# Kernel tuning notes

Hardware: AMD Instinct MI355X
Metric: run time of the kernel (lower is better)

Reference implementation:

```python
import jax, jax.numpy as jnp
import numpy as np

DIM = 512
HEADS = 8
DIM_HEAD = 64
HIDDEN = HEADS * DIM_HEAD  # 512
B, N, M = 4, 2048, 2048


def setup_inputs() -> dict:
    key = jax.random.key(0)
    ks = jax.random.split(key, 7)
    s = 0.02
    return {
        "x": jax.random.normal(ks[0], (B, N, DIM), jnp.float32),
        "context": jax.random.normal(ks[1], (B, M, DIM), jnp.float32),
        "Wq": jax.random.normal(ks[2], (DIM, HIDDEN), jnp.float32) * s,
        "Wk": jax.random.normal(ks[3], (DIM, HIDDEN), jnp.float32) * s,
        "Wv": jax.random.normal(ks[4], (DIM, HIDDEN), jnp.float32) * s,
        "Wo": jax.random.normal(ks[5], (HIDDEN, DIM), jnp.float32) * s,
        "bo": jnp.zeros((DIM,), jnp.float32),
    }


def reference(x, context, Wq, Wk, Wv, Wo, bo):
    scale = DIM_HEAD ** (-0.5)
    # projections: [B, N, HIDDEN] -> [B, H, N, D]
    def split_heads(t):
        b, n, _ = t.shape
        return t.reshape(b, n, HEADS, DIM_HEAD).transpose(0, 2, 1, 3)
    q = split_heads(x @ Wq)
    k = split_heads(context @ Wk)
    v = split_heads(context @ Wv)
    # scores: [B, H, N, M]
    sim = jnp.einsum('bhid,bhjd->bhij', q, k) * scale
    attn = jax.nn.softmax(sim, axis=-1)
    out = jnp.einsum('bhij,bhjd->bhid', attn, v)  # [B, H, N, D]
    out = out.transpose(0, 2, 1, 3).reshape(x.shape[0], x.shape[1], HIDDEN)
    return out @ Wo + bo
```

## Files before the change

kernel.cpp:

```cpp
#include <hip/hip_runtime.h>
#include <hip/hip_bf16.h>


typedef __attribute__((ext_vector_type(8))) short bf16x8;
typedef __attribute__((ext_vector_type(4))) float f32x4;

#define MFMA16(a, b, c) __builtin_amdgcn_mfma_f32_16x16x32_bf16(a, b, c, 0, 0, 0)
#define SCALE_LOG2E 0.18033688011112042f

static __device__ inline unsigned short f2b(float f) {
    __hip_bfloat16 h = __float2bfloat16(f);
    return __builtin_bit_cast(unsigned short, h);
}
static __device__ inline unsigned int pk_rnd(float hi, float lo) {
    unsigned uh = __builtin_bit_cast(unsigned, hi) + 0x8000u;
    unsigned ul = __builtin_bit_cast(unsigned, lo) + 0x8000u;
    return __builtin_amdgcn_perm(uh, ul, 0x07060302);
}
static __device__ inline void gll16(const void* g, void* l) {
    __builtin_amdgcn_global_load_lds(
        (const __attribute__((address_space(1))) void*)g,
        (__attribute__((address_space(3))) void*)l, 16, 0, 0);
}

__global__ __launch_bounds__(256) void prep_kernel(const float* __restrict__ x,
                                                   const float* __restrict__ ctx,
                                                   const float* __restrict__ Wq,
                                                   const float* __restrict__ Wk,
                                                   const float* __restrict__ Wv,
                                                   const float* __restrict__ Wo,
                                                   unsigned short* __restrict__ xb,
                                                   unsigned short* __restrict__ cb,
                                                   unsigned short* __restrict__ wt_base) {
    __shared__ float T[64][65];
    const int bid = blockIdx.x, tid = threadIdx.x;
    if (bid < 8192) {
        const float* src = (bid < 4096) ? x : ctx;
        unsigned short* dst = (bid < 4096) ? xb : cb;
        int i = (bid & 4095) * 256 + tid;
        const float4 v = reinterpret_cast<const float4*>(src)[i];
        uint2 o;
        o.x = pk_rnd(v.y, v.x);
        o.y = pk_rnd(v.w, v.z);
        reinterpret_cast<uint2*>(dst)[i] = o;
        return;
    }
    const int b = bid - 8192;
    const int which = b >> 6, t6 = b & 63;
    const float* W = (which == 0) ? Wq : (which == 1) ? Wk : (which == 2) ? Wv : Wo;
    unsigned short* Wt = wt_base + (size_t)which * 512 * 512;
    const int n0 = (t6 & 7) * 64, k0 = (t6 >> 3) * 64;
    const int rr = tid >> 4, cc = (tid & 15) * 4;
    #pragma unroll
    for (int i = 0; i < 4; i++) {
        const float4 v = *reinterpret_cast<const float4*>(&W[(size_t)(k0 + rr + 16 * i) * 512 + n0 + cc]);
        T[rr + 16 * i][cc + 0] = v.x; T[rr + 16 * i][cc + 1] = v.y;
        T[rr + 16 * i][cc + 2] = v.z; T[rr + 16 * i][cc + 3] = v.w;
    }
    __syncthreads();
    #pragma unroll
    for (int i = 0; i < 4; i++) {
        int n = rr + 16 * i;
        uint2 o;
        o.x = pk_rnd(T[cc + 1][n], T[cc + 0][n]);
        o.y = pk_rnd(T[cc + 3][n], T[cc + 2][n]);
        *reinterpret_cast<uint2*>(&Wt[(size_t)(n0 + n) * 512 + k0 + cc]) = o;
    }
}

__device__ inline void gemm_tile_128(const unsigned short* __restrict__ A,
                                     const unsigned short* __restrict__ Bt,
                                     int row0, int col0, f32x4 acc[4][4]) {
    __shared__ unsigned short As[128 * 32];
    __shared__ unsigned short Bs[128 * 32];
    const int tid  = threadIdx.x;
    const int lane = tid & 63, wave = tid >> 6;
    const int quad = lane >> 4, mr = lane & 15;
    const int m_off = (wave & 1) * 64, n_off = (wave >> 1) * 64;

    const int lrow = lane >> 2;
    const int lq   = (lane & 3) ^ (lrow & 3);
    const unsigned short* aSrc = A  + (size_t)(row0 + wave * 32 + lrow) * 512 + lq * 8;
    const unsigned short* bSrc = Bt + (size_t)(col0 + wave * 32 + lrow) * 512 + lq * 8;
    unsigned short* aL0 = &As[(wave * 32) * 32];
    unsigned short* aL1 = &As[(wave * 32 + 16) * 32];
    unsigned short* bL0 = &Bs[(wave * 32) * 32];
    unsigned short* bL1 = &Bs[(wave * 32 + 16) * 32];

    for (int kt = 0; kt < 16; kt++) {
        __syncthreads();
        gll16(aSrc + kt * 32, aL0);
        gll16(aSrc + 16 * 512 + kt * 32, aL1);
        gll16(bSrc + kt * 32, bL0);
        gll16(bSrc + 16 * 512 + kt * 32, bL1);
        __syncthreads();
        bf16x8 af[4], bfr[4];
        #pragma unroll
        for (int i = 0; i < 4; i++) {
            int m = m_off + i * 16 + mr;
            af[i] = *reinterpret_cast<const bf16x8*>(&As[m * 32 + ((quad ^ (m & 3)) * 8)]);
        }
        #pragma unroll
        for (int j = 0; j < 4; j++) {
            int n = n_off + j * 16 + mr;
            bfr[j] = *reinterpret_cast<const bf16x8*>(&Bs[n * 32 + ((quad ^ (n & 3)) * 8)]);
        }
        #pragma unroll
        for (int i = 0; i < 4; i++)
            #pragma unroll
            for (int j = 0; j < 4; j++)
                acc[i][j] = MFMA16(af[i], bfr[j], acc[i][j]);
    }
}

__global__ __launch_bounds__(256) void gemm_proj_kernel(const unsigned short* __restrict__ xb,
                                                        const unsigned short* __restrict__ cb,
                                                        const unsigned short* __restrict__ wt_base,
                                                        unsigned short* __restrict__ qkv_base) {
    const int f = blockIdx.x, g = f & 7, j = f >> 3;
    const int xt = j & 3;
    const int ry = g + 8 * ((j >> 2) & 7);
    const int which = j >> 5;

    const unsigned short* A  = (which == 0) ? xb : cb;
    const unsigned short* Bt = wt_base + (size_t)which * 512 * 512;
    unsigned short* out      = qkv_base + (size_t)which * 8192 * 512;

    f32x4 acc[4][4];
    #pragma unroll
    for (int i = 0; i < 4; i++)
        #pragma unroll
        for (int j2 = 0; j2 < 4; j2++) acc[i][j2] = (f32x4){0.f, 0.f, 0.f, 0.f};

    gemm_tile_128(A, Bt, ry * 128, xt * 128, acc);

    const int lane = threadIdx.x & 63, wave = threadIdx.x >> 6;
    const int quad = lane >> 4, mr = lane & 15;
    const int m_off = (wave & 1) * 64, n_off = (wave >> 1) * 64;
    const float qs = (which == 0) ? SCALE_LOG2E : 1.0f;

    if (which == 2) {
        #pragma unroll
        for (int i = 0; i < 4; i++) {
            #pragma unroll
            for (int j2 = 0; j2 < 4; j2++) {
                int gcol = xt * 128 + n_off + j2 * 16 + mr;
                int h = gcol >> 6, d = gcol & 63;
                #pragma unroll
                for (int r = 0; r < 4; r++) {
                    int grow = ry * 128 + m_off + i * 16 + quad * 4 + r;
                    int b = grow >> 11, n = grow & 2047;
                    out[((size_t)(b * 8 + h) * 64 + d) * 2048 + n] = f2b(acc[i][j2][r]);
                }
            }
        }
    } else {
        #pragma unroll
        for (int i = 0; i < 4; i++) {
            #pragma unroll
            for (int j2 = 0; j2 < 4; j2++) {
                int gcol = xt * 128 + n_off + j2 * 16 + mr;
                int h = gcol >> 6, d = gcol & 63;
                #pragma unroll
                for (int r = 0; r < 4; r++) {
                    int grow = ry * 128 + m_off + i * 16 + quad * 4 + r;
                    int b = grow >> 11, n = grow & 2047;
                    out[((size_t)(b * 8 + h) * 2048 + n) * 64 + d] = f2b(acc[i][j2][r] * qs);
                }
            }
        }
    }
}

__global__ __launch_bounds__(256) void flash_kernel(const unsigned short* __restrict__ qw,
                                                    const unsigned short* __restrict__ kw,
                                                    const unsigned short* __restrict__ vt,
                                                    float* __restrict__ p0,
                                                    float* __restrict__ p1,
                                                    float* __restrict__ l0,
                                                    float* __restrict__ l1) {
    __shared__ unsigned short Ks[64 * 72];
    __shared__ unsigned short Vs[64 * 72];
    __shared__ unsigned short Pw[4][32 * 72];

    const int f = blockIdx.x, g = f & 7, j = f >> 3;
    const int qtile = j & 15;
    const int kidx  = (j >> 4) & 1;
    const int bh    = g + 8 * (j >> 5);

    const int tid  = threadIdx.x;
    const int lane = tid & 63, wave = tid >> 6;
    const int quad = lane >> 4, mr = lane & 15;

    const unsigned short* qbase = qw + ((size_t)bh * 2048 + qtile * 128 + wave * 32) * 64;
    const unsigned short* kbase = kw + (size_t)bh * 2048 * 64;
    const unsigned short* vbase = vt + (size_t)bh * 64 * 2048;
    float* Pdst = kidx ? p1 : p0;
    float* ldst = kidx ? l1 : l0;

    bf16x8 qf[2][2];
    #pragma unroll
    for (int gq = 0; gq < 2; gq++) {
        qf[gq][0] = *reinterpret_cast<const bf16x8*>(qbase + (gq * 16 + mr) * 64 + quad * 8);
        qf[gq][1] = *reinterpret_cast<const bf16x8*>(qbase + (gq * 16 + mr) * 64 + 32 + quad * 8);
    }

    bf16x8 ones;
    #pragma unroll
    for (int e = 0; e < 8; e++) ones[e] = (short)0x3F80;

    f32x4 oacc[2][4], lacc[2];
    #pragma unroll
    for (int gq = 0; gq < 2; gq++) {
        lacc[gq] = (f32x4){0.f, 0.f, 0.f, 0.f};
        #pragma unroll
        for (int nt = 0; nt < 4; nt++) oacc[gq][nt] = (f32x4){0.f, 0.f, 0.f, 0.f};
    }

    const int srow = tid >> 2, soff = (tid & 3) * 16;

    const int kbeg = kidx * 1024;
    for (int key0 = kbeg; key0 < kbeg + 1024; key0 += 64) {
        __syncthreads();
        {
            const uint4* kp = reinterpret_cast<const uint4*>(kbase + (size_t)(key0 + srow) * 64 + soff);
            uint4* kd = reinterpret_cast<uint4*>(&Ks[srow * 72 + soff]);
            kd[0] = kp[0]; kd[1] = kp[1];
            const uint4* vp = reinterpret_cast<const uint4*>(vbase + (size_t)srow * 2048 + key0 + soff);
            uint4* vd = reinterpret_cast<uint4*>(&Vs[srow * 72 + soff]);
            vd[0] = vp[0]; vd[1] = vp[1];
        }
        __syncthreads();

        f32x4 sv[2][4];
        #pragma unroll
        for (int gq = 0; gq < 2; gq++)
            #pragma unroll
            for (int kt = 0; kt < 4; kt++) sv[gq][kt] = (f32x4){0.f, 0.f, 0.f, 0.f};
        #pragma unroll
        for (int c = 0; c < 2; c++) {
            #pragma unroll
            for (int kt = 0; kt < 4; kt++) {
                bf16x8 kf = *reinterpret_cast<const bf16x8*>(&Ks[(kt * 16 + mr) * 72 + c * 32 + quad * 8]);
                sv[0][kt] = MFMA16(kf, qf[0][c], sv[0][kt]);
                sv[1][kt] = MFMA16(kf, qf[1][c], sv[1][kt]);
            }
        }

        #pragma unroll
        for (int gq = 0; gq < 2; gq++) {
            #pragma unroll
            for (int kt = 0; kt < 4; kt++) {
                uint2 w;
                w.x = pk_rnd(__builtin_exp2f(sv[gq][kt][1]), __builtin_exp2f(sv[gq][kt][0]));
                w.y = pk_rnd(__builtin_exp2f(sv[gq][kt][3]), __builtin_exp2f(sv[gq][kt][2]));
                *reinterpret_cast<uint2*>(&Pw[wave][(gq * 16 + mr) * 72 + kt * 16 + quad * 4]) = w;
            }
        }
        asm volatile("s_waitcnt lgkmcnt(0)" ::: "memory");

        #pragma unroll
        for (int ks = 0; ks < 2; ks++) {
            bf16x8 pf0 = *reinterpret_cast<const bf16x8*>(&Pw[wave][(mr) * 72 + ks * 32 + quad * 8]);
            bf16x8 pf1 = *reinterpret_cast<const bf16x8*>(&Pw[wave][(16 + mr) * 72 + ks * 32 + quad * 8]);
            lacc[0] = MFMA16(pf0, ones, lacc[0]);
            lacc[1] = MFMA16(pf1, ones, lacc[1]);
            #pragma unroll
            for (int nt = 0; nt < 4; nt++) {
                bf16x8 vf = *reinterpret_cast<const bf16x8*>(&Vs[(nt * 16 + mr) * 72 + ks * 32 + quad * 8]);
                oacc[0][nt] = MFMA16(pf0, vf, oacc[0][nt]);
                oacc[1][nt] = MFMA16(pf1, vf, oacc[1][nt]);
            }
        }
    }

    const int b = bh >> 3, h = bh & 7;
    #pragma unroll
    for (int gq = 0; gq < 2; gq++) {
        #pragma unroll
        for (int nt = 0; nt < 4; nt++) {
            #pragma unroll
            for (int r = 0; r < 4; r++) {
                int row = qtile * 128 + wave * 32 + gq * 16 + quad * 4 + r;
                Pdst[((size_t)b * 2048 + row) * 512 + h * 64 + nt * 16 + mr] = oacc[gq][nt][r];
            }
        }
        if (mr == 0) {
            #pragma unroll
            for (int r = 0; r < 4; r++) {
                int row = qtile * 128 + wave * 32 + gq * 16 + quad * 4 + r;
                ldst[(size_t)bh * 2048 + row] = lacc[gq][r];
            }
        }
    }
}

__global__ __launch_bounds__(256) void combine_kernel(const float* __restrict__ p0,
                                                      const float* __restrict__ p1,
                                                      const float* __restrict__ l0,
                                                      const float* __restrict__ l1,
                                                      unsigned short* __restrict__ ob) {
    const int idx = blockIdx.x * 256 + threadIdx.x;
    const size_t flat = (size_t)idx * 4;
    const int row = (int)(flat >> 9);
    const int c   = (int)(flat & 511);
    const int bh  = (row >> 11) * 8 + (c >> 6);
    const int qn  = row & 2047;
    const float lv = l0[(size_t)bh * 2048 + qn] + l1[(size_t)bh * 2048 + qn];
    const float li = 1.0f / lv;
    const float4 a = reinterpret_cast<const float4*>(p0)[idx];
    const float4 bb = reinterpret_cast<const float4*>(p1)[idx];
    uint2 o;
    o.x = pk_rnd((a.y + bb.y) * li, (a.x + bb.x) * li);
    o.y = pk_rnd((a.w + bb.w) * li, (a.z + bb.z) * li);
    reinterpret_cast<uint2*>(ob)[idx] = o;
}

__global__ __launch_bounds__(256) void gemm_out_kernel(const unsigned short* __restrict__ obuf,
                                                       const unsigned short* __restrict__ Wot,
                                                       const float* __restrict__ bo,
                                                       float* __restrict__ out) {
    const int f = blockIdx.x, g = f & 7, j = f >> 3;
    const int xt = j & 3;
    const int ry = g + 8 * (j >> 2);

    f32x4 acc[4][4];
    #pragma unroll
    for (int i = 0; i < 4; i++)
        #pragma unroll
        for (int j2 = 0; j2 < 4; j2++) acc[i][j2] = (f32x4){0.f, 0.f, 0.f, 0.f};

    gemm_tile_128(obuf, Wot, ry * 128, xt * 128, acc);

    const int lane = threadIdx.x & 63, wave = threadIdx.x >> 6;
    const int quad = lane >> 4, mr = lane & 15;
    const int m_off = (wave & 1) * 64, n_off = (wave >> 1) * 64;
    #pragma unroll
    for (int i = 0; i < 4; i++) {
        #pragma unroll
        for (int j2 = 0; j2 < 4; j2++) {
            int gcol = xt * 128 + n_off + j2 * 16 + mr;
            float bias = bo[gcol];
            #pragma unroll
            for (int r = 0; r < 4; r++) {
                int grow = ry * 128 + m_off + i * 16 + quad * 4 + r;
                out[(size_t)grow * 512 + gcol] = acc[i][j2][r] + bias;
            }
        }
    }
}

extern "C" void kernel_launch(void* const* d_in, const int* in_sizes, int n_in,
                              void* d_out, int out_size, void* d_ws, size_t ws_size,
                              hipStream_t stream) {
    const float* x   = (const float*)d_in[0];
    const float* ctx = (const float*)d_in[1];
    const float* Wq  = (const float*)d_in[2];
    const float* Wk  = (const float*)d_in[3];
    const float* Wv  = (const float*)d_in[4];
    const float* Wo  = (const float*)d_in[5];
    const float* bo  = (const float*)d_in[6];
    float* out = (float*)d_out;

    unsigned short* ws  = (unsigned short*)d_ws;
    unsigned short* xb  = ws;
    unsigned short* cb  = xb + (size_t)8192 * 512;
    unsigned short* Wt  = cb + (size_t)8192 * 512;
    unsigned short* qkv = Wt + (size_t)4 * 512 * 512;
    unsigned short* ob  = qkv + (size_t)3 * 8192 * 512;

    float* p0 = out;
    float* p1 = (float*)xb;
    float* l0 = (float*)Wt;
    float* l1 = (float*)(Wt + (size_t)512 * 512);

    prep_kernel<<<8448, 256, 0, stream>>>(x, ctx, Wq, Wk, Wv, Wo, xb, cb, Wt);
    gemm_proj_kernel<<<768, 256, 0, stream>>>(xb, cb, Wt, qkv);
    flash_kernel<<<1024, 256, 0, stream>>>(qkv, qkv + (size_t)8192 * 512,
                                           qkv + (size_t)2 * 8192 * 512, p0, p1, l0, l1);
    combine_kernel<<<4096, 256, 0, stream>>>(p0, p1, l0, l1, ob);
    gemm_out_kernel<<<256, 256, 0, stream>>>(ob, Wt + (size_t)3 * 512 * 512, bo, out);
}
```

Measured before the change: 194.5 us.

## Load K/V fragments directly from global into registers, drop LDS staging and barriers

The flash kernel no longer stages K and V tiles through shared memory with two barriers per iteration. Each wave now loads its own MFMA fragments straight from global memory into registers, and a minimum-occupancy hint is added to the launch bounds. Separately, the V-transpose projection epilogue packs four bf16 values into one 8-byte store instead of four scalar stores. The loader change removes block-wide synchronisation and LDS traffic, but each of the four waves now re-reads the same K/V data from global memory or cache and raises register pressure.

```diff
diff --git a/kernel.cpp b/kernel.cpp
--- a/kernel.cpp
+++ b/kernel.cpp
@@ -146,12 +146,12 @@
             for (int j2 = 0; j2 < 4; j2++) {
                 int gcol = xt * 128 + n_off + j2 * 16 + mr;
                 int h = gcol >> 6, d = gcol & 63;
-                #pragma unroll
-                for (int r = 0; r < 4; r++) {
-                    int grow = ry * 128 + m_off + i * 16 + quad * 4 + r;
-                    int b = grow >> 11, n = grow & 2047;
-                    out[((size_t)(b * 8 + h) * 64 + d) * 2048 + n] = f2b(acc[i][j2][r]);
-                }
+                int grow = ry * 128 + m_off + i * 16 + quad * 4;
+                int b = grow >> 11, n = grow & 2047;
+                uint2 o;
+                o.x = pk_rnd(acc[i][j2][1], acc[i][j2][0]);
+                o.y = pk_rnd(acc[i][j2][3], acc[i][j2][2]);
+                *reinterpret_cast<uint2*>(&out[((size_t)(b * 8 + h) * 64 + d) * 2048 + n]) = o;
             }
         }
     } else {
@@ -172,15 +172,13 @@
     }
 }
 
-__global__ __launch_bounds__(256) void flash_kernel(const unsigned short* __restrict__ qw,
-                                                    const unsigned short* __restrict__ kw,
-                                                    const unsigned short* __restrict__ vt,
-                                                    float* __restrict__ p0,
-                                                    float* __restrict__ p1,
-                                                    float* __restrict__ l0,
-                                                    float* __restrict__ l1) {
-    __shared__ unsigned short Ks[64 * 72];
-    __shared__ unsigned short Vs[64 * 72];
+__global__ __launch_bounds__(256, 4) void flash_kernel(const unsigned short* __restrict__ qw,
+                                                       const unsigned short* __restrict__ kw,
+                                                       const unsigned short* __restrict__ vt,
+                                                       float* __restrict__ p0,
+                                                       float* __restrict__ p1,
+                                                       float* __restrict__ l0,
+                                                       float* __restrict__ l1) {
     __shared__ unsigned short Pw[4][32 * 72];
 
     const int f = blockIdx.x, g = f & 7, j = f >> 3;
@@ -193,8 +191,8 @@
     const int quad = lane >> 4, mr = lane & 15;
 
     const unsigned short* qbase = qw + ((size_t)bh * 2048 + qtile * 128 + wave * 32) * 64;
-    const unsigned short* kbase = kw + (size_t)bh * 2048 * 64;
-    const unsigned short* vbase = vt + (size_t)bh * 64 * 2048;
+    const unsigned short* kL = kw + (size_t)bh * 2048 * 64 + (size_t)mr * 64 + quad * 8;
+    const unsigned short* vL = vt + (size_t)bh * 64 * 2048 + (size_t)mr * 2048 + quad * 8;
     float* Pdst = kidx ? p1 : p0;
     float* ldst = kidx ? l1 : l0;
 
@@ -217,20 +215,21 @@
         for (int nt = 0; nt < 4; nt++) oacc[gq][nt] = (f32x4){0.f, 0.f, 0.f, 0.f};
     }
 
-    const int srow = tid >> 2, soff = (tid & 3) * 16;
-
     const int kbeg = kidx * 1024;
     for (int key0 = kbeg; key0 < kbeg + 1024; key0 += 64) {
-        __syncthreads();
-        {
-            const uint4* kp = reinterpret_cast<const uint4*>(kbase + (size_t)(key0 + srow) * 64 + soff);
-            uint4* kd = reinterpret_cast<uint4*>(&Ks[srow * 72 + soff]);
-            kd[0] = kp[0]; kd[1] = kp[1];
-            const uint4* vp = reinterpret_cast<const uint4*>(vbase + (size_t)srow * 2048 + key0 + soff);
-            uint4* vd = reinterpret_cast<uint4*>(&Vs[srow * 72 + soff]);
-            vd[0] = vp[0]; vd[1] = vp[1];
-        }
-        __syncthreads();
+        bf16x8 kf[2][4];
+        #pragma unroll
+        for (int c = 0; c < 2; c++)
+            #pragma unroll
+            for (int kt = 0; kt < 4; kt++)
+                kf[c][kt] = *reinterpret_cast<const bf16x8*>(kL + (size_t)(key0 + kt * 16) * 64 + c * 32);
+
+        bf16x8 vf[2][4];
+        #pragma unroll
+        for (int ks = 0; ks < 2; ks++)
+            #pragma unroll
+            for (int nt = 0; nt < 4; nt++)
+                vf[ks][nt] = *reinterpret_cast<const bf16x8*>(vL + (size_t)nt * 16 * 2048 + key0 + ks * 32);
 
         f32x4 sv[2][4];
         #pragma unroll
@@ -241,9 +240,8 @@
         for (int c = 0; c < 2; c++) {
             #pragma unroll
             for (int kt = 0; kt < 4; kt++) {
-                bf16x8 kf = *reinterpret_cast<const bf16x8*>(&Ks[(kt * 16 + mr) * 72 + c * 32 + quad * 8]);
-                sv[0][kt] = MFMA16(kf, qf[0][c], sv[0][kt]);
-                sv[1][kt] = MFMA16(kf, qf[1][c], sv[1][kt]);
+                sv[0][kt] = MFMA16(kf[c][kt], qf[0][c], sv[0][kt]);
+                sv[1][kt] = MFMA16(kf[c][kt], qf[1][c], sv[1][kt]);
             }
         }
 
@@ -267,9 +265,8 @@
             lacc[1] = MFMA16(pf1, ones, lacc[1]);
             #pragma unroll
             for (int nt = 0; nt < 4; nt++) {
-                bf16x8 vf = *reinterpret_cast<const bf16x8*>(&Vs[(nt * 16 + mr) * 72 + ks * 32 + quad * 8]);
-                oacc[0][nt] = MFMA16(pf0, vf, oacc[0][nt]);
-                oacc[1][nt] = MFMA16(pf1, vf, oacc[1][nt]);
+                oacc[0][nt] = MFMA16(pf0, vf[ks][nt], oacc[0][nt]);
+                oacc[1][nt] = MFMA16(pf1, vf[ks][nt], oacc[1][nt]);
             }
         }
     }
```

Result: slower. 272.7 us (+40.2%).
